# Kernel tuning notes

Measured on AMD Instinct MI355X. Metric: run time of the kernel, lower is better.

Reference implementation:

```python
import jax, jax.numpy as jnp
import numpy as np

V, H, B, T = 100000, 512, 4096, 524288
EPS = 1e-5

def setup_inputs() -> dict:
    key = jax.random.key(0)
    ks = jax.random.split(key, 8)
    tokens = jax.random.randint(ks[0], (T,), 0, V, dtype=jnp.int32)
    seg_ids = jnp.sort(jax.random.randint(ks[1], (T,), 0, B, dtype=jnp.int32))
    t = jax.random.bernoulli(ks[2], 0.5, (B,)).astype(jnp.float32)
    emb = jax.random.normal(ks[3], (V, H), dtype=jnp.float32) * 0.1
    W1 = jax.random.normal(ks[4], (H, H), dtype=jnp.float32) * (1.0 / np.sqrt(H))
    b1 = jnp.zeros((H,), jnp.float32)
    gamma = jnp.ones((H,), jnp.float32)
    beta = jnp.zeros((H,), jnp.float32)
    w2 = jax.random.normal(ks[5], (H,), dtype=jnp.float32) * (1.0 / np.sqrt(H))
    b2 = jnp.zeros((), jnp.float32)
    return {"tokens": tokens, "seg_ids": seg_ids, "t": t, "emb": emb,
            "W1": W1, "b1": b1, "gamma": gamma, "beta": beta, "w2": w2, "b2": b2}

def reference(tokens, seg_ids, t, emb, W1, b1, gamma, beta, w2, b2):
    nb = t.shape[0]
    # fused gather + segment-mean (bag-of-words), replaces the per-sample loop
    gathered = emb[tokens]  # [T, H]
    sums = jax.ops.segment_sum(gathered, seg_ids, num_segments=nb)  # [B, H]
    counts = jax.ops.segment_sum(jnp.ones((tokens.shape[0],), jnp.float32), seg_ids, num_segments=nb)
    bow = sums / jnp.maximum(counts, 1.0)[:, None]  # [B, H]
    # Linear -> BatchNorm1d (training-mode batch stats, biased var) -> ReLU
    z = bow @ W1.T + b1  # [B, H]
    mu = jnp.mean(z, axis=0)
    var = jnp.mean((z - mu) ** 2, axis=0)
    zn = (z - mu) * jax.lax.rsqrt(var + EPS) * gamma + beta
    h = jax.nn.relu(zn)  # dropout treated as identity (eval mode) for determinism
    logits = h @ w2 + b2  # [B]
    # BCEWithLogitsLoss: mean(softplus(logit) - t*logit), numerically stable
    loss = jnp.mean(jnp.logaddexp(0.0, logits) - t * logits)
    return (loss, logits)
```

## Files before the change

### kernel.cpp

```cpp
#include <hip/hip_runtime.h>
#include <hip/hip_bf16.h>
#include <hip/hip_fp16.h>
#include <math.h>

constexpr int NTOK = 524288;
constexpr int NB   = 4096;
constexpr int H    = 512;
constexpr float EPS = 1e-5f;

struct h4 { __half2 a, b; };

__global__ __launch_bounds__(256) void k_convert(
    const float* __restrict__ emb, h4* __restrict__ embh) {
  size_t i = (size_t)blockIdx.x * 256 + threadIdx.x;
  float4 v = ((const float4*)emb)[i];
  h4 o;
  o.a = __floats2half2_rn(v.x, v.y);
  o.b = __floats2half2_rn(v.z, v.w);
  embh[i] = o;
}

__global__ __launch_bounds__(256) void k_gather_mean(
    const int* __restrict__ tokens, const int* __restrict__ seg,
    const h4* __restrict__ embh, float* __restrict__ bow) {
  const int b = blockIdx.x;
  int lo = 0, hi = NTOK;
  while (lo < hi) { int mid = (lo + hi) >> 1; if (seg[mid] < b) lo = mid + 1; else hi = mid; }
  const int start = lo;
  hi = NTOK;
  while (lo < hi) { int mid = (lo + hi) >> 1; if (seg[mid] < b + 1) lo = mid + 1; else hi = mid; }
  const int end = lo;

  const int tid = threadIdx.x;
  const int col = tid & 127;
  const int g = tid >> 7;

  float4 acc = make_float4(0.f, 0.f, 0.f, 0.f);
  int i = start + g;
  for (; i + 6 < end; i += 8) {
    int t0 = tokens[i], t1 = tokens[i + 2], t2 = tokens[i + 4], t3 = tokens[i + 6];
    h4 v0 = embh[(size_t)t0 * 128 + col];
    h4 v1 = embh[(size_t)t1 * 128 + col];
    h4 v2 = embh[(size_t)t2 * 128 + col];
    h4 v3 = embh[(size_t)t3 * 128 + col];
    float2 a0 = __half22float2(v0.a), b0 = __half22float2(v0.b);
    float2 a1 = __half22float2(v1.a), b1 = __half22float2(v1.b);
    float2 a2 = __half22float2(v2.a), b2 = __half22float2(v2.b);
    float2 a3 = __half22float2(v3.a), b3 = __half22float2(v3.b);
    acc.x += a0.x + a1.x + a2.x + a3.x;
    acc.y += a0.y + a1.y + a2.y + a3.y;
    acc.z += b0.x + b1.x + b2.x + b3.x;
    acc.w += b0.y + b1.y + b2.y + b3.y;
  }
  for (; i < end; i += 2) {
    h4 v0 = embh[(size_t)tokens[i] * 128 + col];
    float2 a0 = __half22float2(v0.a), b0 = __half22float2(v0.b);
    acc.x += a0.x; acc.y += a0.y; acc.z += b0.x; acc.w += b0.y;
  }

  __shared__ float4 part[128];
  if (g == 1) part[col] = acc;
  __syncthreads();
  if (g == 0) {
    float4 p = part[col];
    const int cnt = end - start;
    const float s = 1.0f / (float)(cnt > 0 ? cnt : 1);
    acc.x = (acc.x + p.x) * s; acc.y = (acc.y + p.y) * s;
    acc.z = (acc.z + p.z) * s; acc.w = (acc.w + p.w) * s;
    ((float4*)bow)[(size_t)b * 128 + col] = acc;
  }
}

constexpr int BM = 64, BN = 64, BK = 32;
constexpr int LST = BM + 4;

__global__ __launch_bounds__(256) void k_gemm(
    const float* __restrict__ A, const float* __restrict__ W,
    const float* __restrict__ b1, float* __restrict__ C) {
  __shared__ float As[BK][LST];
  __shared__ float Bs[BK][LST];
  const int tid = threadIdx.x;
  const int tx = tid & 15, ty = tid >> 4;
  const int bm0 = blockIdx.x * BM;
  const int bn0 = blockIdx.y * BN;

  const int lrow = tid >> 3;
  const int lc4  = (tid & 7) * 4;

  float acc[4][4] = {};

  for (int kc = 0; kc < H; kc += BK) {
    float4 a0 = *(const float4*)&A[(size_t)(bm0 + lrow)      * H + kc + lc4];
    float4 a1 = *(const float4*)&A[(size_t)(bm0 + lrow + 32) * H + kc + lc4];
    float4 w0 = *(const float4*)&W[(size_t)(bn0 + lrow)      * H + kc + lc4];
    float4 w1 = *(const float4*)&W[(size_t)(bn0 + lrow + 32) * H + kc + lc4];
    __syncthreads();
    As[lc4 + 0][lrow] = a0.x; As[lc4 + 1][lrow] = a0.y;
    As[lc4 + 2][lrow] = a0.z; As[lc4 + 3][lrow] = a0.w;
    As[lc4 + 0][lrow + 32] = a1.x; As[lc4 + 1][lrow + 32] = a1.y;
    As[lc4 + 2][lrow + 32] = a1.z; As[lc4 + 3][lrow + 32] = a1.w;
    Bs[lc4 + 0][lrow] = w0.x; Bs[lc4 + 1][lrow] = w0.y;
    Bs[lc4 + 2][lrow] = w0.z; Bs[lc4 + 3][lrow] = w0.w;
    Bs[lc4 + 0][lrow + 32] = w1.x; Bs[lc4 + 1][lrow + 32] = w1.y;
    Bs[lc4 + 2][lrow + 32] = w1.z; Bs[lc4 + 3][lrow + 32] = w1.w;
    __syncthreads();
#pragma unroll
    for (int k = 0; k < BK; ++k) {
      float4 av = *(const float4*)&As[k][ty * 4];
      float4 bv = *(const float4*)&Bs[k][tx * 4];
      acc[0][0] += av.x * bv.x; acc[0][1] += av.x * bv.y; acc[0][2] += av.x * bv.z; acc[0][3] += av.x * bv.w;
      acc[1][0] += av.y * bv.x; acc[1][1] += av.y * bv.y; acc[1][2] += av.y * bv.z; acc[1][3] += av.y * bv.w;
      acc[2][0] += av.z * bv.x; acc[2][1] += av.z * bv.y; acc[2][2] += av.z * bv.z; acc[2][3] += av.z * bv.w;
      acc[3][0] += av.w * bv.x; acc[3][1] += av.w * bv.y; acc[3][2] += av.w * bv.z; acc[3][3] += av.w * bv.w;
    }
  }
  const float4 bb = *(const float4*)&b1[bn0 + tx * 4];
#pragma unroll
  for (int i = 0; i < 4; ++i) {
    float4 o;
    o.x = acc[i][0] + bb.x; o.y = acc[i][1] + bb.y;
    o.z = acc[i][2] + bb.z; o.w = acc[i][3] + bb.w;
    *(float4*)&C[(size_t)(bm0 + ty * 4 + i) * H + bn0 + tx * 4] = o;
  }
}

__global__ __launch_bounds__(256) void k_colstats(
    const float* __restrict__ z, float* __restrict__ ps, float* __restrict__ pss) {
  const int blk = blockIdx.x;
  const int c0 = threadIdx.x * 2;
  const int r0 = blk * 64;
  float s0 = 0, s1 = 0, q0 = 0, q1 = 0;
  for (int r = 0; r < 64; ++r) {
    float2 v = *(const float2*)&z[(size_t)(r0 + r) * H + c0];
    s0 += v.x; s1 += v.y;
    q0 += v.x * v.x; q1 += v.y * v.y;
  }
  ps[blk * H + c0] = s0; ps[blk * H + c0 + 1] = s1;
  pss[blk * H + c0] = q0; pss[blk * H + c0 + 1] = q1;
}

__global__ __launch_bounds__(512) void k_finalize(
    const float* __restrict__ ps, const float* __restrict__ pss,
    const float* __restrict__ gamma, const float* __restrict__ beta,
    float* __restrict__ scale, float* __restrict__ shift) {
  const int c = threadIdx.x;
  float s = 0, q = 0;
  for (int i = 0; i < 64; ++i) { s += ps[i * H + c]; q += pss[i * H + c]; }
  const float mu = s * (1.0f / NB);
  const float var = q * (1.0f / NB) - mu * mu;
  const float rstd = rsqrtf(var + EPS);
  const float sc = rstd * gamma[c];
  scale[c] = sc;
  shift[c] = beta[c] - mu * sc;
}

__global__ __launch_bounds__(256) void k_bn_dot(
    const float* __restrict__ z, const float* __restrict__ scale,
    const float* __restrict__ shift, const float* __restrict__ w2,
    const float* __restrict__ b2, float* __restrict__ out) {
  const int tid = threadIdx.x;
  const int wave = tid >> 6, lane = tid & 63;
  const int b = blockIdx.x * 4 + wave;
  const float4* __restrict__ z4 = (const float4*)(z + (size_t)b * H);
  const float4* __restrict__ sc4 = (const float4*)scale;
  const float4* __restrict__ sh4 = (const float4*)shift;
  const float4* __restrict__ w24 = (const float4*)w2;
  float acc = 0.f;
#pragma unroll
  for (int i = lane; i < 128; i += 64) {
    float4 zv = z4[i], sc = sc4[i], sh = sh4[i], w = w24[i];
    float h0 = fmaxf(zv.x * sc.x + sh.x, 0.f);
    float h1 = fmaxf(zv.y * sc.y + sh.y, 0.f);
    float h2 = fmaxf(zv.z * sc.z + sh.z, 0.f);
    float h3 = fmaxf(zv.w * sc.w + sh.w, 0.f);
    acc += h0 * w.x + h1 * w.y + h2 * w.z + h3 * w.w;
  }
#pragma unroll
  for (int off = 32; off > 0; off >>= 1) acc += __shfl_down(acc, off, 64);
  if (lane == 0) out[1 + b] = acc + b2[0];
}

__global__ __launch_bounds__(256) void k_loss(
    const float* __restrict__ t, float* __restrict__ d_out) {
  const int tid = threadIdx.x;
  float s = 0.f;
  for (int b = tid; b < NB; b += 256) {
    float x = d_out[1 + b];
    float sp = fmaxf(x, 0.f) + log1pf(expf(-fabsf(x)));
    s += sp - t[b] * x;
  }
  __shared__ float red[256];
  red[tid] = s;
  __syncthreads();
  for (int off = 128; off > 0; off >>= 1) {
    if (tid < off) red[tid] += red[tid + off];
    __syncthreads();
  }
  if (tid == 0) d_out[0] = red[0] * (1.0f / NB);
}

extern "C" void kernel_launch(void* const* d_in, const int* in_sizes, int n_in,
                              void* d_out, int out_size, void* d_ws, size_t ws_size,
                              hipStream_t stream) {
  const int*   tokens = (const int*)d_in[0];
  const int*   seg    = (const int*)d_in[1];
  const float* t      = (const float*)d_in[2];
  const float* emb    = (const float*)d_in[3];
  const float* W1     = (const float*)d_in[4];
  const float* b1     = (const float*)d_in[5];
  const float* gamma  = (const float*)d_in[6];
  const float* beta   = (const float*)d_in[7];
  const float* w2     = (const float*)d_in[8];
  const float* b2     = (const float*)d_in[9];
  float* out = (float*)d_out;

  char* wsb = (char*)d_ws;
  h4*    embh  = (h4*)wsb;
  float* bow   = (float*)(wsb + 102400000);
  float* z     = bow + (size_t)NB * H;
  float* ps    = z + (size_t)NB * H;
  float* pss   = ps + 64 * H;
  float* scale = pss + 64 * H;
  float* shift = scale + H;

  k_convert<<<50000, 256, 0, stream>>>(emb, embh);
  k_gather_mean<<<NB, 256, 0, stream>>>(tokens, seg, embh, bow);
  dim3 ggrid(NB / BM, H / BN);
  k_gemm<<<ggrid, 256, 0, stream>>>(bow, W1, b1, z);
  k_colstats<<<64, 256, 0, stream>>>(z, ps, pss);
  k_finalize<<<1, 512, 0, stream>>>(ps, pss, gamma, beta, scale, shift);
  k_bn_dot<<<NB / 4, 256, 0, stream>>>(z, scale, shift, w2, b2, out);
  k_loss<<<1, 256, 0, stream>>>(t, out);
}
```

Baseline: 445.9 us.

## Use fp16 MFMA for the linear layer and widen gather loads

Stores the bag-of-words mean in fp16 and converts W1 to fp16 so the dense layer runs on MFMA 16x16x32 instructions with one wave per 16x64 output tile. The gather now reads 16-byte half8 vectors per lane with four token groups per block. Finalize and loss kernels are relaunched with different block shapes. This reduces GEMM compute cost and gather instruction count, at the cost of fp16 rounding of the bow activations and an extra conversion launch.

```diff
diff --git a/kernel.cpp b/kernel.cpp
--- a/kernel.cpp
+++ b/kernel.cpp
@@ -8,21 +8,23 @@
 constexpr int H    = 512;
 constexpr float EPS = 1e-5f;
 
+typedef _Float16 half8 __attribute__((ext_vector_type(8)));
+typedef float f32x4 __attribute__((ext_vector_type(4)));
 struct h4 { __half2 a, b; };
 
 __global__ __launch_bounds__(256) void k_convert(
-    const float* __restrict__ emb, h4* __restrict__ embh) {
+    const float* __restrict__ src, h4* __restrict__ dst) {
   size_t i = (size_t)blockIdx.x * 256 + threadIdx.x;
-  float4 v = ((const float4*)emb)[i];
+  float4 v = ((const float4*)src)[i];
   h4 o;
   o.a = __floats2half2_rn(v.x, v.y);
   o.b = __floats2half2_rn(v.z, v.w);
-  embh[i] = o;
+  dst[i] = o;
 }
 
 __global__ __launch_bounds__(256) void k_gather_mean(
     const int* __restrict__ tokens, const int* __restrict__ seg,
-    const h4* __restrict__ embh, float* __restrict__ bow) {
+    const half8* __restrict__ embh, half8* __restrict__ bow_h) {
   const int b = blockIdx.x;
   int lo = 0, hi = NTOK;
   while (lo < hi) { int mid = (lo + hi) >> 1; if (seg[mid] < b) lo = mid + 1; else hi = mid; }
@@ -32,95 +34,84 @@
   const int end = lo;
 
   const int tid = threadIdx.x;
-  const int col = tid & 127;
-  const int g = tid >> 7;
-
-  float4 acc = make_float4(0.f, 0.f, 0.f, 0.f);
+  const int lane = tid & 63;
+  const int g = tid >> 6;
+
+  float acc[8] = {};
   int i = start + g;
-  for (; i + 6 < end; i += 8) {
-    int t0 = tokens[i], t1 = tokens[i + 2], t2 = tokens[i + 4], t3 = tokens[i + 6];
-    h4 v0 = embh[(size_t)t0 * 128 + col];
-    h4 v1 = embh[(size_t)t1 * 128 + col];
-    h4 v2 = embh[(size_t)t2 * 128 + col];
-    h4 v3 = embh[(size_t)t3 * 128 + col];
-    float2 a0 = __half22float2(v0.a), b0 = __half22float2(v0.b);
-    float2 a1 = __half22float2(v1.a), b1 = __half22float2(v1.b);
-    float2 a2 = __half22float2(v2.a), b2 = __half22float2(v2.b);
-    float2 a3 = __half22float2(v3.a), b3 = __half22float2(v3.b);
-    acc.x += a0.x + a1.x + a2.x + a3.x;
-    acc.y += a0.y + a1.y + a2.y + a3.y;
-    acc.z += b0.x + b1.x + b2.x + b3.x;
-    acc.w += b0.y + b1.y + b2.y + b3.y;
-  }
-  for (; i < end; i += 2) {
-    h4 v0 = embh[(size_t)tokens[i] * 128 + col];
-    float2 a0 = __half22float2(v0.a), b0 = __half22float2(v0.b);
-    acc.x += a0.x; acc.y += a0.y; acc.z += b0.x; acc.w += b0.y;
-  }
-
-  __shared__ float4 part[128];
-  if (g == 1) part[col] = acc;
+  for (; i + 12 < end; i += 16) {
+    half8 v0 = embh[(size_t)tokens[i]      * 64 + lane];
+    half8 v1 = embh[(size_t)tokens[i + 4]  * 64 + lane];
+    half8 v2 = embh[(size_t)tokens[i + 8]  * 64 + lane];
+    half8 v3 = embh[(size_t)tokens[i + 12] * 64 + lane];
+#pragma unroll
+    for (int j = 0; j < 8; ++j)
+      acc[j] += (float)v0[j] + (float)v1[j] + (float)v2[j] + (float)v3[j];
+  }
+  for (; i < end; i += 4) {
+    half8 v0 = embh[(size_t)tokens[i] * 64 + lane];
+#pragma unroll
+    for (int j = 0; j < 8; ++j) acc[j] += (float)v0[j];
+  }
+
+  __shared__ float part[3][64][9];
+  if (g > 0) {
+#pragma unroll
+    for (int j = 0; j < 8; ++j) part[g - 1][lane][j] = acc[j];
+  }
   __syncthreads();
   if (g == 0) {
-    float4 p = part[col];
     const int cnt = end - start;
     const float s = 1.0f / (float)(cnt > 0 ? cnt : 1);
-    acc.x = (acc.x + p.x) * s; acc.y = (acc.y + p.y) * s;
-    acc.z = (acc.z + p.z) * s; acc.w = (acc.w + p.w) * s;
-    ((float4*)bow)[(size_t)b * 128 + col] = acc;
-  }
-}
-
-constexpr int BM = 64, BN = 64, BK = 32;
-constexpr int LST = BM + 4;
-
-__global__ __launch_bounds__(256) void k_gemm(
-    const float* __restrict__ A, const float* __restrict__ W,
+    half8 o;
+#pragma unroll
+    for (int j = 0; j < 8; ++j) {
+      float v = acc[j] + part[0][lane][j] + part[1][lane][j] + part[2][lane][j];
+      o[j] = (_Float16)(v * s);
+    }
+    bow_h[(size_t)b * 64 + lane] = o;
+  }
+}
+
+__global__ __launch_bounds__(256) void k_gemm_mfma(
+    const _Float16* __restrict__ A,
+    const _Float16* __restrict__ Bw,
     const float* __restrict__ b1, float* __restrict__ C) {
-  __shared__ float As[BK][LST];
-  __shared__ float Bs[BK][LST];
-  const int tid = threadIdx.x;
-  const int tx = tid & 15, ty = tid >> 4;
-  const int bm0 = blockIdx.x * BM;
-  const int bn0 = blockIdx.y * BN;
-
-  const int lrow = tid >> 3;
-  const int lc4  = (tid & 7) * 4;
-
-  float acc[4][4] = {};
-
-  for (int kc = 0; kc < H; kc += BK) {
-    float4 a0 = *(const float4*)&A[(size_t)(bm0 + lrow)      * H + kc + lc4];
-    float4 a1 = *(const float4*)&A[(size_t)(bm0 + lrow + 32) * H + kc + lc4];
-    float4 w0 = *(const float4*)&W[(size_t)(bn0 + lrow)      * H + kc + lc4];
-    float4 w1 = *(const float4*)&W[(size_t)(bn0 + lrow + 32) * H + kc + lc4];
-    __syncthreads();
-    As[lc4 + 0][lrow] = a0.x; As[lc4 + 1][lrow] = a0.y;
-    As[lc4 + 2][lrow] = a0.z; As[lc4 + 3][lrow] = a0.w;
-    As[lc4 + 0][lrow + 32] = a1.x; As[lc4 + 1][lrow + 32] = a1.y;
-    As[lc4 + 2][lrow + 32] = a1.z; As[lc4 + 3][lrow + 32] = a1.w;
-    Bs[lc4 + 0][lrow] = w0.x; Bs[lc4 + 1][lrow] = w0.y;
-    Bs[lc4 + 2][lrow] = w0.z; Bs[lc4 + 3][lrow] = w0.w;
-    Bs[lc4 + 0][lrow + 32] = w1.x; Bs[lc4 + 1][lrow + 32] = w1.y;
-    Bs[lc4 + 2][lrow + 32] = w1.z; Bs[lc4 + 3][lrow + 32] = w1.w;
-    __syncthreads();
-#pragma unroll
-    for (int k = 0; k < BK; ++k) {
-      float4 av = *(const float4*)&As[k][ty * 4];
-      float4 bv = *(const float4*)&Bs[k][tx * 4];
-      acc[0][0] += av.x * bv.x; acc[0][1] += av.x * bv.y; acc[0][2] += av.x * bv.z; acc[0][3] += av.x * bv.w;
-      acc[1][0] += av.y * bv.x; acc[1][1] += av.y * bv.y; acc[1][2] += av.y * bv.z; acc[1][3] += av.y * bv.w;
-      acc[2][0] += av.z * bv.x; acc[2][1] += av.z * bv.y; acc[2][2] += av.z * bv.z; acc[2][3] += av.z * bv.w;
-      acc[3][0] += av.w * bv.x; acc[3][1] += av.w * bv.y; acc[3][2] += av.w * bv.z; acc[3][3] += av.w * bv.w;
-    }
-  }
-  const float4 bb = *(const float4*)&b1[bn0 + tx * 4];
-#pragma unroll
-  for (int i = 0; i < 4; ++i) {
-    float4 o;
-    o.x = acc[i][0] + bb.x; o.y = acc[i][1] + bb.y;
-    o.z = acc[i][2] + bb.z; o.w = acc[i][3] + bb.w;
-    *(float4*)&C[(size_t)(bm0 + ty * 4 + i) * H + bn0 + tx * 4] = o;
+  const int tid = threadIdx.x;
+  const int lane = tid & 63;
+  const int gw = blockIdx.x * 4 + (tid >> 6);
+  const int m0 = (gw >> 3) * 16;
+  const int n0 = (gw & 7) * 64;
+  const int l15 = lane & 15, quad = lane >> 4;
+
+  f32x4 acc0 = {}, acc1 = {}, acc2 = {}, acc3 = {};
+  const _Float16* ap = A + (size_t)(m0 + l15) * H + quad * 8;
+  const _Float16* bp = Bw + (size_t)(n0 + l15) * H + quad * 8;
+
+#pragma unroll
+  for (int k = 0; k < H; k += 32) {
+    half8 af  = *(const half8*)(ap + k);
+    half8 bf0 = *(const half8*)(bp + k);
+    half8 bf1 = *(const half8*)(bp + 16 * H + k);
+    half8 bf2 = *(const half8*)(bp + 32 * H + k);
+    half8 bf3 = *(const half8*)(bp + 48 * H + k);
+    acc0 = __builtin_amdgcn_mfma_f32_16x16x32_f16(af, bf0, acc0, 0, 0, 0);
+    acc1 = __builtin_amdgcn_mfma_f32_16x16x32_f16(af, bf1, acc1, 0, 0, 0);
+    acc2 = __builtin_amdgcn_mfma_f32_16x16x32_f16(af, bf2, acc2, 0, 0, 0);
+    acc3 = __builtin_amdgcn_mfma_f32_16x16x32_f16(af, bf3, acc3, 0, 0, 0);
+  }
+
+  const float bn0v = b1[n0 + l15];
+  const float bn1v = b1[n0 + 16 + l15];
+  const float bn2v = b1[n0 + 32 + l15];
+  const float bn3v = b1[n0 + 48 + l15];
+  float* crow = C + (size_t)(m0 + quad * 4) * H + n0 + l15;
+#pragma unroll
+  for (int r = 0; r < 4; ++r) {
+    crow[(size_t)r * H]      = acc0[r] + bn0v;
+    crow[(size_t)r * H + 16] = acc1[r] + bn1v;
+    crow[(size_t)r * H + 32] = acc2[r] + bn2v;
+    crow[(size_t)r * H + 48] = acc3[r] + bn3v;
   }
 }
 
@@ -139,12 +130,13 @@
   pss[blk * H + c0] = q0; pss[blk * H + c0 + 1] = q1;
 }
 
-__global__ __launch_bounds__(512) void k_finalize(
+__global__ __launch_bounds__(128) void k_finalize(
     const float* __restrict__ ps, const float* __restrict__ pss,
     const float* __restrict__ gamma, const float* __restrict__ beta,
     float* __restrict__ scale, float* __restrict__ shift) {
-  const int c = threadIdx.x;
+  const int c = blockIdx.x * 128 + threadIdx.x;
   float s = 0, q = 0;
+#pragma unroll 8
   for (int i = 0; i < 64; ++i) { s += ps[i * H + c]; q += pss[i * H + c]; }
   const float mu = s * (1.0f / NB);
   const float var = q * (1.0f / NB) - mu * mu;
@@ -180,19 +172,20 @@
   if (lane == 0) out[1 + b] = acc + b2[0];
 }
 
-__global__ __launch_bounds__(256) void k_loss(
+__global__ __launch_bounds__(1024) void k_loss(
     const float* __restrict__ t, float* __restrict__ d_out) {
   const int tid = threadIdx.x;
   float s = 0.f;
-  for (int b = tid; b < NB; b += 256) {
+#pragma unroll
+  for (int b = tid; b < NB; b += 1024) {
     float x = d_out[1 + b];
     float sp = fmaxf(x, 0.f) + log1pf(expf(-fabsf(x)));
     s += sp - t[b] * x;
   }
-  __shared__ float red[256];
+  __shared__ float red[1024];
   red[tid] = s;
   __syncthreads();
-  for (int off = 128; off > 0; off >>= 1) {
+  for (int off = 512; off > 0; off >>= 1) {
     if (tid < off) red[tid] += red[tid + off];
     __syncthreads();
   }
@@ -215,20 +208,21 @@
   float* out = (float*)d_out;
 
   char* wsb = (char*)d_ws;
-  h4*    embh  = (h4*)wsb;
-  float* bow   = (float*)(wsb + 102400000);
-  float* z     = bow + (size_t)NB * H;
-  float* ps    = z + (size_t)NB * H;
-  float* pss   = ps + 64 * H;
-  float* scale = pss + 64 * H;
-  float* shift = scale + H;
-
-  k_convert<<<50000, 256, 0, stream>>>(emb, embh);
-  k_gather_mean<<<NB, 256, 0, stream>>>(tokens, seg, embh, bow);
-  dim3 ggrid(NB / BM, H / BN);
-  k_gemm<<<ggrid, 256, 0, stream>>>(bow, W1, b1, z);
+  half8*    embh  = (half8*)wsb;
+  _Float16* W1h   = (_Float16*)(wsb + 102400000);
+  half8*    bow_h = (half8*)(wsb + 102924288);
+  float*    z     = (float*)(wsb + 107118592);
+  float*    ps    = (float*)(wsb + 115507200);
+  float*    pss   = ps + 64 * H;
+  float*    scale = pss + 64 * H;
+  float*    shift = scale + H;
+
+  k_convert<<<50000, 256, 0, stream>>>(emb, (h4*)embh);
+  k_convert<<<256, 256, 0, stream>>>(W1, (h4*)W1h);
+  k_gather_mean<<<NB, 256, 0, stream>>>(tokens, seg, embh, bow_h);
+  k_gemm_mfma<<<512, 256, 0, stream>>>((const _Float16*)bow_h, W1h, b1, z);
   k_colstats<<<64, 256, 0, stream>>>(z, ps, pss);
-  k_finalize<<<1, 512, 0, stream>>>(ps, pss, gamma, beta, scale, shift);
+  k_finalize<<<4, 128, 0, stream>>>(ps, pss, gamma, beta, scale, shift);
   k_bn_dot<<<NB / 4, 256, 0, stream>>>(z, scale, shift, w2, b2, out);
-  k_loss<<<1, 256, 0, stream>>>(t, out);
-}
+  k_loss<<<1, 1024, 0, stream>>>(t, out);
+}
```

Result: faster. 420.3 us (-5.7%).
